# Kernel tuning notes

Measured on AMD Instinct MI355X. Metric: run time of the kernel, lower is better.

## Reference

```python
import jax, jax.numpy as jnp
import numpy as np

N = 100000      # nodes
E = 3200000     # edges (before self loops)
IN = 128        # in_channels
H = 8           # heads
C = 16          # out_channels per head
NEG_SLOPE = 0.2


def setup_inputs() -> dict:
    key = jax.random.key(0)
    k1, k2, k3, k4, k5, k6 = jax.random.split(key, 6)
    x = jax.random.normal(k1, (N, IN), dtype=jnp.float32)
    edge_index = jax.random.randint(k2, (2, E), 0, N, dtype=jnp.int32)
    # GATConv params: lin weight [IN, H*C], att_src/att_dst [H, C], bias [H*C]
    W = jax.random.normal(k3, (IN, H * C), dtype=jnp.float32) / np.float32(np.sqrt(IN))
    att_src = jax.random.normal(k4, (H, C), dtype=jnp.float32) / np.float32(np.sqrt(C))
    att_dst = jax.random.normal(k5, (H, C), dtype=jnp.float32) / np.float32(np.sqrt(C))
    bias = jax.random.normal(k6, (H * C,), dtype=jnp.float32) * 0.01
    return {"x": x, "edge_index": edge_index, "W": W,
            "att_src": att_src, "att_dst": att_dst, "bias": bias}


def reference(x, edge_index, W, att_src, att_dst, bias):
    n = x.shape[0]
    h = (x @ W).reshape(n, H, C)                      # [N, H, C]
    # add self loops (PyG default add_self_loops=True)
    loop = jnp.arange(n, dtype=edge_index.dtype)
    src = jnp.concatenate([edge_index[0], loop])      # [E+N] message sources j
    dst = jnp.concatenate([edge_index[1], loop])      # [E+N] targets i
    # per-node attention logits
    a_src = jnp.einsum('nhc,hc->nh', h, att_src)      # [N, H]
    a_dst = jnp.einsum('nhc,hc->nh', h, att_dst)      # [N, H]
    alpha = jax.nn.leaky_relu(a_src[src] + a_dst[dst], NEG_SLOPE)  # [E+N, H]
    # segment softmax over edges grouped by destination node
    amax = jax.lax.stop_gradient(jax.ops.segment_max(alpha, dst, num_segments=n))
    ex = jnp.exp(alpha - amax[dst])
    denom = jax.ops.segment_sum(ex, dst, num_segments=n)           # [N, H]
    w = ex / (denom[dst] + 1e-16)                                  # [E+N, H]
    msg = h[src] * w[:, :, None]                                   # [E+N, H, C]
    out = jax.ops.segment_sum(msg, dst, num_segments=n)            # [N, H, C]
    return out.reshape(n, H * C) + bias
```

## Files before the change

### kernel.cpp

```cpp
#include <hip/hip_runtime.h>
#include <hip/hip_bf16.h>

#define H 8
#define C 16
#define HC 128
#define NEG 0.2f
#define XS_S 132

#define ANSH 6
#define AN 64
#define AMSK 63
#define CAP2 2560
#define MAXB2 2048
#define CB_SH 12
#define CBMSK 4095
#define MAXB1 64
#define EPB 8192

__device__ __forceinline__ float lrelu(float x) { return fmaxf(x, NEG * x); }

__device__ __forceinline__ unsigned pack_bf16(float a, float b) {
    union { __hip_bfloat16 h; unsigned short u; } ua, ub;
    ua.h = __float2bfloat16(a);
    ub.h = __float2bfloat16(b);
    return (unsigned)ua.u | ((unsigned)ub.u << 16);
}
__device__ __forceinline__ float bf_lo(unsigned d) { return __uint_as_float(d << 16); }
__device__ __forceinline__ float bf_hi(unsigned d) { return __uint_as_float(d & 0xffff0000u); }

__global__ void __launch_bounds__(256) k1_gemm(const float* __restrict__ x,
                                               const float* __restrict__ W,
                                               const float* __restrict__ att_src,
                                               const float* __restrict__ att_dst,
                                               unsigned* __restrict__ h16,
                                               float* __restrict__ a_src,
                                               float* __restrict__ a_dst, int N) {
    __shared__ float xs[64 * XS_S];
    const int n0 = blockIdx.x * 64;
    const int t = threadIdx.x;
#pragma unroll
    for (int i = 0; i < 8; ++i) {
        int id = t + 256 * i;
        int r = id >> 5, kq = id & 31;
        int n = n0 + r;
        float4 v = (n < N) ? ((const float4*)x)[(size_t)n * 32 + kq]
                           : make_float4(0.f, 0.f, 0.f, 0.f);
        *(float4*)&xs[r * XS_S + kq * 4] = v;
    }
    __syncthreads();
    const int cg = t & 31;
    const int r0 = (t >> 5) * 8;
    float acc[8][4];
#pragma unroll
    for (int i = 0; i < 8; ++i)
#pragma unroll
        for (int j = 0; j < 4; ++j) acc[i][j] = 0.f;

#pragma unroll 4
    for (int k = 0; k < HC; ++k) {
        const float4 wv = ((const float4*)W)[k * 32 + cg];
        float wr[4] = {wv.x, wv.y, wv.z, wv.w};
#pragma unroll
        for (int i = 0; i < 8; ++i) {
            float xv = xs[(r0 + i) * XS_S + k];
#pragma unroll
            for (int j = 0; j < 4; ++j) acc[i][j] += xv * wr[j];
        }
    }
    const int fhd = cg >> 2;
    const int cq  = cg & 3;
#pragma unroll
    for (int i = 0; i < 8; ++i) {
        int n = n0 + r0 + i;
        if (n < N) {
            uint2 dv = make_uint2(pack_bf16(acc[i][0], acc[i][1]),
                                  pack_bf16(acc[i][2], acc[i][3]));
            *(uint2*)&h16[(size_t)n * 64 + cg * 2] = dv;
        }
        float ps = 0.f, pd = 0.f;
#pragma unroll
        for (int jj = 0; jj < 4; ++jj) {
            float hv = acc[i][jj];
            ps += hv * att_src[fhd * C + cq * 4 + jj];
            pd += hv * att_dst[fhd * C + cq * 4 + jj];
        }
        ps += __shfl_xor(ps, 1, 4); pd += __shfl_xor(pd, 1, 4);
        ps += __shfl_xor(ps, 2, 4); pd += __shfl_xor(pd, 2, 4);
        if (cq == 0 && n < N) {
            a_src[(unsigned)n * 8u + fhd] = ps;
            a_dst[(unsigned)n * 8u + fhd] = pd;
        }
    }
}

__global__ void __launch_bounds__(512) kb_bin1(const int* __restrict__ ei,
                                               int* __restrict__ gcount1,
                                               unsigned* __restrict__ pairs1,
                                               int E, int NB1, int cap1) {
    __shared__ unsigned sp[EPB];
    __shared__ int cnt[MAXB1];
    __shared__ int scn[MAXB1];
    __shared__ int gbase[MAXB1];
    const int t = threadIdx.x;
    const int e0 = blockIdx.x * EPB;
    const int nE = min(EPB, E - e0);
    if (t < MAXB1) cnt[t] = 0;
    __syncthreads();

    const bool v4 = ((E & 3) == 0) && ((nE & 3) == 0);
    const int nE4 = nE >> 2;
    const int4* d4p = (const int4*)(ei + E + e0);
    const int4* s4p = (const int4*)(ei + e0);
    if (v4) {
        for (int i = t; i < nE4; i += 512) {
            int4 d = d4p[i];
            atomicAdd(&cnt[d.x >> CB_SH], 1);
            atomicAdd(&cnt[d.y >> CB_SH], 1);
            atomicAdd(&cnt[d.z >> CB_SH], 1);
            atomicAdd(&cnt[d.w >> CB_SH], 1);
        }
    } else {
        for (int i = t; i < nE; i += 512)
            atomicAdd(&cnt[ei[E + e0 + i] >> CB_SH], 1);
    }
    __syncthreads();
    if (t < MAXB1) scn[t] = cnt[t];
    __syncthreads();
    for (int off = 1; off < MAXB1; off <<= 1) {
        int v = (t < MAXB1 && t >= off) ? scn[t - off] : 0;
        __syncthreads();
        if (t < MAXB1) scn[t] += v;
        __syncthreads();
    }
    if (t < MAXB1) {
        int h = cnt[t];
        gbase[t] = h ? t * cap1 + atomicAdd(&gcount1[t], h) : 0;
        cnt[t] = scn[t] - h;
    }
    __syncthreads();
    if (v4) {
        for (int i = t; i < nE4; i += 512) {
            int4 d = d4p[i];
            int4 sv = s4p[i];
#pragma unroll
            for (int q = 0; q < 4; ++q) {
                int dst = (&d.x)[q], src = (&sv.x)[q];
                int pos = atomicAdd(&cnt[dst >> CB_SH], 1);
                sp[pos] = (unsigned)src | ((unsigned)(dst & CBMSK) << 17);
            }
        }
    } else {
        for (int i = t; i < nE; i += 512) {
            int dst = ei[E + e0 + i], src = ei[e0 + i];
            int pos = atomicAdd(&cnt[dst >> CB_SH], 1);
            sp[pos] = (unsigned)src | ((unsigned)(dst & CBMSK) << 17);
        }
    }
    __syncthreads();
    const int wv = t >> 6, lane = t & 63;
    for (int i = wv; i < NB1; i += 8) {
        int end = scn[i];
        int st  = (i > 0) ? scn[i - 1] : 0;
        int len = end - st;
        if (len <= 0) continue;
        int gb = gbase[i];
        int rem = i * cap1 + cap1 - gb;
        int wl = min(len, max(rem, 0));
        for (int k = lane; k < wl; k += 64)
            pairs1[gb + k] = sp[st + k];
    }
}

__global__ void __launch_bounds__(512) kb_bin2(const unsigned* __restrict__ pairs1,
                                               const int* __restrict__ gcount1,
                                               int* __restrict__ gcount2,
                                               unsigned* __restrict__ pairs2,
                                               int cap1, int ch2) {
    __shared__ unsigned sp[EPB];
    __shared__ int cnt[64];
    __shared__ int scn[64];
    __shared__ int gbase[64];
    const int cb = blockIdx.x / ch2;
    const int ci = blockIdx.x % ch2;
    const int c1 = min(gcount1[cb], cap1);
    const int e0 = ci * EPB;
    if (e0 >= c1) return;
    const int nE = min(EPB, c1 - e0);
    const unsigned b1 = (unsigned)cb * (unsigned)cap1 + (unsigned)e0;
    const int t = threadIdx.x;
    if (t < 64) cnt[t] = 0;
    __syncthreads();

    const int nE4 = nE >> 2;
    const uint4* p4 = (const uint4*)(pairs1 + b1);
    for (int i = t; i < nE4; i += 512) {
        uint4 p = p4[i];
        atomicAdd(&cnt[p.x >> 23], 1);
        atomicAdd(&cnt[p.y >> 23], 1);
        atomicAdd(&cnt[p.z >> 23], 1);
        atomicAdd(&cnt[p.w >> 23], 1);
    }
    for (int i = (nE4 << 2) + t; i < nE; i += 512)
        atomicAdd(&cnt[pairs1[b1 + i] >> 23], 1);
    __syncthreads();
    if (t < 64) scn[t] = cnt[t];
    __syncthreads();
    for (int off = 1; off < 64; off <<= 1) {
        int v = (t < 64 && t >= off) ? scn[t - off] : 0;
        __syncthreads();
        if (t < 64) scn[t] += v;
        __syncthreads();
    }
    if (t < 64) {
        int h = cnt[t];
        int gfb = cb * 64 + t;
        gbase[t] = h ? gfb * CAP2 + atomicAdd(&gcount2[gfb], h) : 0;
        cnt[t] = scn[t] - h;
    }
    __syncthreads();
    for (int i = t; i < nE4; i += 512) {
        uint4 p = p4[i];
#pragma unroll
        for (int q = 0; q < 4; ++q) {
            unsigned pv = (&p.x)[q];
            int pos = atomicAdd(&cnt[pv >> 23], 1);
            sp[pos] = (pv & 0x1FFFFu) | (((pv >> 17) & 63u) << 18);
        }
    }
    for (int i = (nE4 << 2) + t; i < nE; i += 512) {
        unsigned pv = pairs1[b1 + i];
        int pos = atomicAdd(&cnt[pv >> 23], 1);
        sp[pos] = (pv & 0x1FFFFu) | (((pv >> 17) & 63u) << 18);
    }
    __syncthreads();
    const int wv = t >> 6, lane = t & 63;
    for (int i = wv; i < 64; i += 8) {
        int end = scn[i];
        int st  = (i > 0) ? scn[i - 1] : 0;
        int len = end - st;
        if (len <= 0) continue;
        int gb = gbase[i];
        int fb0 = (cb * 64 + i) * CAP2;
        int rem = fb0 + CAP2 - gb;
        int wl = min(len, max(rem, 0));
        for (int k = lane; k < wl; k += 64)
            pairs2[gb + k] = sp[st + k];
    }
}

__global__ void __launch_bounds__(512) k_fused(const unsigned* __restrict__ pairs,
                                               const int* __restrict__ gcount,
                                               const unsigned* __restrict__ h16,
                                               const float* __restrict__ a_src,
                                               const float* __restrict__ a_dst,
                                               const float* __restrict__ bias,
                                               float* __restrict__ out, int N) {
    __shared__ int cnt[AN];
    __shared__ int sc[AN];
    __shared__ int lcur[AN];
    __shared__ int lbeg[AN + 1];
    __shared__ unsigned scol[CAP2];
    const int b = blockIdx.x;
    const int t = threadIdx.x;
    const int n0 = b << ANSH;
    const unsigned base = (unsigned)b * (unsigned)CAP2;
    const int cb = min(gcount[b], CAP2);

    if (t < AN) cnt[t] = 0;
    __syncthreads();
    for (int j = t; j < cb; j += 512)
        atomicAdd(&cnt[pairs[base + j] >> 18], 1);
    __syncthreads();
    if (t < AN) sc[t] = cnt[t];
    __syncthreads();
    for (int off = 1; off < AN; off <<= 1) {
        int v = (t < AN && t >= off) ? sc[t - off] : 0;
        __syncthreads();
        if (t < AN) sc[t] += v;
        __syncthreads();
    }
    if (t < AN) {
        lbeg[t + 1] = sc[t];
        lcur[t] = sc[t] - cnt[t];
        if (t == 0) lbeg[0] = 0;
    }
    __syncthreads();
    for (int j = t; j < cb; j += 512) {
        unsigned pv = pairs[base + j];
        int pos = atomicAdd(&lcur[pv >> 18], 1);
        scol[pos] = pv & 0x3FFFFu;
    }
    __syncthreads();

    const int wv = t >> 6;
    const int lane = t & 63;
    const int hd = lane >> 3;
    const int hw = lane & 7;
    const int bidx = hd * 4;

    for (int nl = wv; nl < AN; nl += 8) {
        const int node = n0 + nl;
        if (node >= N) break;
        const float adst_own = a_dst[(unsigned)node * 8u + (unsigned)hd];
        const float adst_hh  = a_dst[(unsigned)node * 8u + (unsigned)hw];
        const float wself = __expf(lrelu(a_src[(unsigned)node * 8u + (unsigned)hd] + adst_own));
        unsigned dself = h16[(unsigned)node * 64u + (unsigned)lane];
        float a0 = bf_lo(dself) * wself, a1 = bf_hi(dself) * wself;
        float b0 = 0.f, b1 = 0.f, c0 = 0.f, c1 = 0.f, e0 = 0.f, e1 = 0.f;
        float sA = wself, sB = 0.f, sC = 0.f, sD = 0.f;

        const int beg = lbeg[nl], end = lbeg[nl + 1];
        int j = beg;
        for (; j + 8 <= end; j += 8) {
            unsigned m0 = scol[j],     m1 = scol[j + 1], m2 = scol[j + 2], m3 = scol[j + 3];
            unsigned m4 = scol[j + 4], m5 = scol[j + 5], m6 = scol[j + 6], m7 = scol[j + 7];
            unsigned nP = scol[j + (lane >> 3)];
            float wme = __expf(lrelu(a_src[nP * 8u + (unsigned)hw] + adst_hh));
            int wi = __float_as_int(wme);
            float w0 = __int_as_float(__builtin_amdgcn_ds_bpermute(bidx,       wi));
            float w1 = __int_as_float(__builtin_amdgcn_ds_bpermute(bidx + 32,  wi));
            float w2 = __int_as_float(__builtin_amdgcn_ds_bpermute(bidx + 64,  wi));
            float w3 = __int_as_float(__builtin_amdgcn_ds_bpermute(bidx + 96,  wi));
            float w4 = __int_as_float(__builtin_amdgcn_ds_bpermute(bidx + 128, wi));
            float w5 = __int_as_float(__builtin_amdgcn_ds_bpermute(bidx + 160, wi));
            float w6 = __int_as_float(__builtin_amdgcn_ds_bpermute(bidx + 192, wi));
            float w7 = __int_as_float(__builtin_amdgcn_ds_bpermute(bidx + 224, wi));
            unsigned d0 = h16[m0 * 64u + (unsigned)lane];
            unsigned d1 = h16[m1 * 64u + (unsigned)lane];
            unsigned d2 = h16[m2 * 64u + (unsigned)lane];
            unsigned d3 = h16[m3 * 64u + (unsigned)lane];
            unsigned d4 = h16[m4 * 64u + (unsigned)lane];
            unsigned d5 = h16[m5 * 64u + (unsigned)lane];
            unsigned d6 = h16[m6 * 64u + (unsigned)lane];
            unsigned d7 = h16[m7 * 64u + (unsigned)lane];
            a0 += bf_lo(d0) * w0; a1 += bf_hi(d0) * w0; sA += w0;
            b0 += bf_lo(d1) * w1; b1 += bf_hi(d1) * w1; sB += w1;
            c0 += bf_lo(d2) * w2; c1 += bf_hi(d2) * w2; sC += w2;
            e0 += bf_lo(d3) * w3; e1 += bf_hi(d3) * w3; sD += w3;
            a0 += bf_lo(d4) * w4; a1 += bf_hi(d4) * w4; sA += w4;
            b0 += bf_lo(d5) * w5; b1 += bf_hi(d5) * w5; sB += w5;
            c0 += bf_lo(d6) * w6; c1 += bf_hi(d6) * w6; sC += w6;
            e0 += bf_lo(d7) * w7; e1 += bf_hi(d7) * w7; sD += w7;
        }
        if (j + 4 <= end) {
            unsigned m0 = scol[j], m1 = scol[j + 1], m2 = scol[j + 2], m3 = scol[j + 3];
            unsigned nP = scol[j + ((lane >> 3) & 3)];
            float wme = __expf(lrelu(a_src[nP * 8u + (unsigned)hw] + adst_hh));
            int wi = __float_as_int(wme);
            float w0 = __int_as_float(__builtin_amdgcn_ds_bpermute(bidx,      wi));
            float w1 = __int_as_float(__builtin_amdgcn_ds_bpermute(bidx + 32, wi));
            float w2 = __int_as_float(__builtin_amdgcn_ds_bpermute(bidx + 64, wi));
            float w3 = __int_as_float(__builtin_amdgcn_ds_bpermute(bidx + 96, wi));
            unsigned d0 = h16[m0 * 64u + (unsigned)lane];
            unsigned d1 = h16[m1 * 64u + (unsigned)lane];
            unsigned d2 = h16[m2 * 64u + (unsigned)lane];
            unsigned d3 = h16[m3 * 64u + (unsigned)lane];
            a0 += bf_lo(d0) * w0; a1 += bf_hi(d0) * w0; sA += w0;
            b0 += bf_lo(d1) * w1; b1 += bf_hi(d1) * w1; sB += w1;
            c0 += bf_lo(d2) * w2; c1 += bf_hi(d2) * w2; sC += w2;
            e0 += bf_lo(d3) * w3; e1 += bf_hi(d3) * w3; sD += w3;
            j += 4;
        }
        for (; j < end; ++j) {
            unsigned mA = scol[j];
            float wA = __expf(lrelu(a_src[mA * 8u + (unsigned)hd] + adst_own));
            unsigned dA = h16[mA * 64u + (unsigned)lane];
            a0 += bf_lo(dA) * wA; a1 += bf_hi(dA) * wA; sA += wA;
        }
        const float s = sA + sB + sC + sD;
        const float inv = 1.f / (s + 1e-16f);
        const float acc0 = a0 + b0 + c0 + e0;
        const float acc1 = a1 + b1 + c1 + e1;
        const float2 bv = ((const float2*)bias)[lane];
        float2 o;
        o.x = acc0 * inv + bv.x;
        o.y = acc1 * inv + bv.y;
        ((float2*)out)[(unsigned)node * 64u + (unsigned)lane] = o;
    }
}

extern "C" void kernel_launch(void* const* d_in, const int* in_sizes, int n_in,
                              void* d_out, int out_size, void* d_ws, size_t ws_size,
                              hipStream_t stream) {
    const float* x       = (const float*)d_in[0];
    const int*   ei      = (const int*)d_in[1];
    const float* W       = (const float*)d_in[2];
    const float* att_src = (const float*)d_in[3];
    const float* att_dst = (const float*)d_in[4];
    const float* bias    = (const float*)d_in[5];
    float* out = (float*)d_out;

    const int N = in_sizes[0] / HC;
    const int E = in_sizes[1] / 2;
    const int B = (N + AMSK) >> ANSH;
    const int NB1 = (N + CBMSK) >> CB_SH;
    const int nbin = (E + EPB - 1) / EPB;
    const int cap1 = (((E + NB1 - 1) / NB1) + 32768 + 3) & ~3;
    const int ch2 = (cap1 + EPB - 1) / EPB;

    unsigned* h16 = (unsigned*)d_ws;
    float* a_src  = (float*)(h16 + (size_t)N * 64);
    float* a_dst  = a_src + (size_t)N * H;
    int* gcount1  = (int*)(a_dst + (size_t)N * H);
    int* gcount2  = gcount1 + MAXB1;
    unsigned* pairs1 = (unsigned*)(gcount2 + MAXB2);
    unsigned* pairs2 = pairs1 + (size_t)NB1 * (size_t)cap1;

    static hipStream_t s_side = nullptr;
    static hipEvent_t ev_fork = nullptr, ev_join = nullptr;
    if (s_side == nullptr) {
        (void)hipStreamCreateWithFlags(&s_side, hipStreamNonBlocking);
        (void)hipEventCreateWithFlags(&ev_fork, hipEventDisableTiming);
        (void)hipEventCreateWithFlags(&ev_join, hipEventDisableTiming);
    }
    const bool fork = (s_side != nullptr && ev_fork != nullptr && ev_join != nullptr);
    hipStream_t sb = fork ? s_side : stream;

    if (fork) {
        (void)hipEventRecord(ev_fork, stream);
        (void)hipStreamWaitEvent(sb, ev_fork, 0);
    }

    (void)hipMemsetAsync(gcount1, 0, (MAXB1 + MAXB2) * sizeof(int), sb);
    kb_bin1<<<nbin, 512, 0, sb>>>(ei, gcount1, pairs1, E, NB1, cap1);
    kb_bin2<<<NB1 * ch2, 512, 0, sb>>>(pairs1, gcount1, gcount2, pairs2,
                                       cap1, ch2);
    if (fork) (void)hipEventRecord(ev_join, sb);

    k1_gemm<<<(N + 63) / 64, 256, 0, stream>>>(x, W, att_src, att_dst,
                                               h16, a_src, a_dst, N);

    if (fork) (void)hipStreamWaitEvent(stream, ev_join, 0);

    k_fused<<<B, 512, 0, stream>>>(pairs2, gcount2, h16, a_src,
                                   a_dst, bias, out, N);
}
```

Baseline: 369.9 us.

## Split bin2 and fused aggregation into groups pipelined across streams

```diff
diff --git a/kernel.cpp b/kernel.cpp
--- a/kernel.cpp
+++ b/kernel.cpp
@@ -16,6 +16,7 @@
 #define CBMSK 4095
 #define MAXB1 64
 #define EPB 8192
+#define NGR 5
 
 __device__ __forceinline__ float lrelu(float x) { return fmaxf(x, NEG * x); }
 
@@ -57,14 +58,20 @@
         for (int j = 0; j < 4; ++j) acc[i][j] = 0.f;
 
 #pragma unroll 4
-    for (int k = 0; k < HC; ++k) {
-        const float4 wv = ((const float4*)W)[k * 32 + cg];
-        float wr[4] = {wv.x, wv.y, wv.z, wv.w};
+    for (int kq = 0; kq < 32; ++kq) {
+        const float4* Wq = (const float4*)W + (kq * 4) * 32 + cg;
+        const float4 wa = Wq[0], wb = Wq[32], wc = Wq[64], wd = Wq[96];
 #pragma unroll
         for (int i = 0; i < 8; ++i) {
-            float xv = xs[(r0 + i) * XS_S + k];
-#pragma unroll
-            for (int j = 0; j < 4; ++j) acc[i][j] += xv * wr[j];
+            const float4 xv = *(const float4*)&xs[(r0 + i) * XS_S + kq * 4];
+            acc[i][0] += xv.x * wa.x; acc[i][1] += xv.x * wa.y;
+            acc[i][2] += xv.x * wa.z; acc[i][3] += xv.x * wa.w;
+            acc[i][0] += xv.y * wb.x; acc[i][1] += xv.y * wb.y;
+            acc[i][2] += xv.y * wb.z; acc[i][3] += xv.y * wb.w;
+            acc[i][0] += xv.z * wc.x; acc[i][1] += xv.z * wc.y;
+            acc[i][2] += xv.z * wc.z; acc[i][3] += xv.z * wc.w;
+            acc[i][0] += xv.w * wd.x; acc[i][1] += xv.w * wd.y;
+            acc[i][2] += xv.w * wd.z; acc[i][3] += xv.w * wd.w;
         }
     }
     const int fhd = cg >> 2;
@@ -175,12 +182,12 @@
                                                const int* __restrict__ gcount1,
                                                int* __restrict__ gcount2,
                                                unsigned* __restrict__ pairs2,
-                                               int cap1, int ch2) {
+                                               int cap1, int ch2, int cb0) {
     __shared__ unsigned sp[EPB];
     __shared__ int cnt[64];
     __shared__ int scn[64];
     __shared__ int gbase[64];
-    const int cb = blockIdx.x / ch2;
+    const int cb = cb0 + blockIdx.x / ch2;
     const int ci = blockIdx.x % ch2;
     const int c1 = min(gcount1[cb], cap1);
     const int e0 = ci * EPB;
@@ -254,13 +261,14 @@
                                                const float* __restrict__ a_src,
                                                const float* __restrict__ a_dst,
                                                const float* __restrict__ bias,
-                                               float* __restrict__ out, int N) {
+                                               float* __restrict__ out,
+                                               int N, int b0) {
     __shared__ int cnt[AN];
     __shared__ int sc[AN];
     __shared__ int lcur[AN];
     __shared__ int lbeg[AN + 1];
     __shared__ unsigned scol[CAP2];
-    const int b = blockIdx.x;
+    const int b = b0 + blockIdx.x;
     const int t = threadIdx.x;
     const int n0 = b << ANSH;
     const unsigned base = (unsigned)b * (unsigned)CAP2;
@@ -306,7 +314,7 @@
         const float wself = __expf(lrelu(a_src[(unsigned)node * 8u + (unsigned)hd] + adst_own));
         unsigned dself = h16[(unsigned)node * 64u + (unsigned)lane];
         float a0 = bf_lo(dself) * wself, a1 = bf_hi(dself) * wself;
-        float b0 = 0.f, b1 = 0.f, c0 = 0.f, c1 = 0.f, e0 = 0.f, e1 = 0.f;
+        float b0_ = 0.f, b1_ = 0.f, c0 = 0.f, c1 = 0.f, e0 = 0.f, e1 = 0.f;
         float sA = wself, sB = 0.f, sC = 0.f, sD = 0.f;
 
         const int beg = lbeg[nl], end = lbeg[nl + 1];
@@ -334,11 +342,11 @@
             unsigned d6 = h16[m6 * 64u + (unsigned)lane];
             unsigned d7 = h16[m7 * 64u + (unsigned)lane];
             a0 += bf_lo(d0) * w0; a1 += bf_hi(d0) * w0; sA += w0;
-            b0 += bf_lo(d1) * w1; b1 += bf_hi(d1) * w1; sB += w1;
+            b0_ += bf_lo(d1) * w1; b1_ += bf_hi(d1) * w1; sB += w1;
             c0 += bf_lo(d2) * w2; c1 += bf_hi(d2) * w2; sC += w2;
             e0 += bf_lo(d3) * w3; e1 += bf_hi(d3) * w3; sD += w3;
             a0 += bf_lo(d4) * w4; a1 += bf_hi(d4) * w4; sA += w4;
-            b0 += bf_lo(d5) * w5; b1 += bf_hi(d5) * w5; sB += w5;
+            b0_ += bf_lo(d5) * w5; b1_ += bf_hi(d5) * w5; sB += w5;
             c0 += bf_lo(d6) * w6; c1 += bf_hi(d6) * w6; sC += w6;
             e0 += bf_lo(d7) * w7; e1 += bf_hi(d7) * w7; sD += w7;
         }
@@ -356,7 +364,7 @@
             unsigned d2 = h16[m2 * 64u + (unsigned)lane];
             unsigned d3 = h16[m3 * 64u + (unsigned)lane];
             a0 += bf_lo(d0) * w0; a1 += bf_hi(d0) * w0; sA += w0;
-            b0 += bf_lo(d1) * w1; b1 += bf_hi(d1) * w1; sB += w1;
+            b0_ += bf_lo(d1) * w1; b1_ += bf_hi(d1) * w1; sB += w1;
             c0 += bf_lo(d2) * w2; c1 += bf_hi(d2) * w2; sC += w2;
             e0 += bf_lo(d3) * w3; e1 += bf_hi(d3) * w3; sD += w3;
             j += 4;
@@ -369,8 +377,8 @@
         }
         const float s = sA + sB + sC + sD;
         const float inv = 1.f / (s + 1e-16f);
-        const float acc0 = a0 + b0 + c0 + e0;
-        const float acc1 = a1 + b1 + c1 + e1;
+        const float acc0 = a0 + b0_ + c0 + e0;
+        const float acc1 = a1 + b1_ + c1 + e1;
         const float2 bv = ((const float2*)bias)[lane];
         float2 o;
         o.x = acc0 * inv + bv.x;
@@ -397,6 +405,7 @@
     const int nbin = (E + EPB - 1) / EPB;
     const int cap1 = (((E + NB1 - 1) / NB1) + 32768 + 3) & ~3;
     const int ch2 = (cap1 + EPB - 1) / EPB;
+    const int gsz = (NB1 + NGR - 1) / NGR;
 
     unsigned* h16 = (unsigned*)d_ws;
     float* a_src  = (float*)(h16 + (size_t)N * 64);
@@ -407,13 +416,16 @@
     unsigned* pairs2 = pairs1 + (size_t)NB1 * (size_t)cap1;
 
     static hipStream_t s_side = nullptr;
-    static hipEvent_t ev_fork = nullptr, ev_join = nullptr;
+    static hipEvent_t ev_fork = nullptr;
+    static hipEvent_t ev2[NGR] = {};
     if (s_side == nullptr) {
         (void)hipStreamCreateWithFlags(&s_side, hipStreamNonBlocking);
         (void)hipEventCreateWithFlags(&ev_fork, hipEventDisableTiming);
-        (void)hipEventCreateWithFlags(&ev_join, hipEventDisableTiming);
-    }
-    const bool fork = (s_side != nullptr && ev_fork != nullptr && ev_join != nullptr);
+        for (int g = 0; g < NGR; ++g)
+            (void)hipEventCreateWithFlags(&ev2[g], hipEventDisableTiming);
+    }
+    bool fork = (s_side != nullptr && ev_fork != nullptr);
+    for (int g = 0; g < NGR; ++g) fork = fork && (ev2[g] != nullptr);
     hipStream_t sb = fork ? s_side : stream;
 
     if (fork) {
@@ -423,15 +435,25 @@
 
     (void)hipMemsetAsync(gcount1, 0, (MAXB1 + MAXB2) * sizeof(int), sb);
     kb_bin1<<<nbin, 512, 0, sb>>>(ei, gcount1, pairs1, E, NB1, cap1);
-    kb_bin2<<<NB1 * ch2, 512, 0, sb>>>(pairs1, gcount1, gcount2, pairs2,
-                                       cap1, ch2);
-    if (fork) (void)hipEventRecord(ev_join, sb);
+    for (int g = 0; g < NGR; ++g) {
+        int cb0 = g * gsz;
+        int ncb = (cb0 < NB1) ? ((NB1 - cb0 < gsz) ? NB1 - cb0 : gsz) : 0;
+        if (ncb > 0)
+            kb_bin2<<<ncb * ch2, 512, 0, sb>>>(pairs1, gcount1, gcount2,
+                                               pairs2, cap1, ch2, cb0);
+        if (fork) (void)hipEventRecord(ev2[g], sb);
+    }
 
     k1_gemm<<<(N + 63) / 64, 256, 0, stream>>>(x, W, att_src, att_dst,
                                                h16, a_src, a_dst, N);
 
-    if (fork) (void)hipStreamWaitEvent(stream, ev_join, 0);
-
-    k_fused<<<B, 512, 0, stream>>>(pairs2, gcount2, h16, a_src,
-                                   a_dst, bias, out, N);
-}
+    for (int g = 0; g < NGR; ++g) {
+        if (fork) (void)hipStreamWaitEvent(stream, ev2[g], 0);
+        int fb0 = (g * gsz) << 6;
+        int fb1 = ((g + 1) * gsz) << 6;
+        if (fb1 > B) fb1 = B;
+        if (fb0 >= fb1) continue;
+        k_fused<<<fb1 - fb0, 512, 0, stream>>>(pairs2, gcount2, h16, a_src,
+                                               a_dst, bias, out, N, fb0);
+    }
+}
```

After: 523.0 us. 41.4% more time.
